# Optimization experiments

Measured on AMD Instinct MI355X. Metric: run time of the kernel, lower is better.

## Reference

```python
import jax, jax.numpy as jnp
import numpy as np

B, S, E, H = 1, 2048, 512, 8
D = E // H
N = B * S
WIN_HALF = 32  # attention_window 64 -> +/-32
ALPHA = 0.1
LN_EPS = 1e-12
NEG_INF = -1e9


def _build_window_edges():
    # windowed graph: dst i attends to src j with |i-j| <= WIN_HALF, within each batch block
    i = np.arange(S)
    offs = np.arange(-WIN_HALF, WIN_HALF + 1)
    src = i[:, None] + offs[None, :]
    dst = np.broadcast_to(i[:, None], src.shape)
    valid = (src >= 0) & (src < S)
    src, dst = src[valid], dst[valid]
    srcs, dsts = [], []
    for b in range(B):
        srcs.append(src + b * S)
        dsts.append(dst + b * S)
    return (np.concatenate(srcs).astype(np.int32),
            np.concatenate(dsts).astype(np.int32))


def setup_inputs() -> dict:
    key = jax.random.key(0)
    ks = jax.random.split(key, 12)
    sc = 1.0 / np.sqrt(E)
    src_np, dst_np = _build_window_edges()
    return {
        "hidden_states": jax.random.normal(ks[0], (B, S, E), dtype=jnp.float32),
        "attention_mask": jnp.zeros((B, S), dtype=jnp.float32),
        "edge_src": jnp.asarray(src_np),
        "edge_dst": jnp.asarray(dst_np),
        "Wq": jax.random.normal(ks[1], (E, E), dtype=jnp.float32) * sc,
        "bq": jnp.zeros((E,), dtype=jnp.float32),
        "Wk": jax.random.normal(ks[2], (E, E), dtype=jnp.float32) * sc,
        "bk": jnp.zeros((E,), dtype=jnp.float32),
        "Wv": jax.random.normal(ks[3], (E, E), dtype=jnp.float32) * sc,
        "bv": jnp.zeros((E,), dtype=jnp.float32),
        "Wo": jax.random.normal(ks[4], (E, E), dtype=jnp.float32) * sc,
        "bo": jnp.zeros((E,), dtype=jnp.float32),
        "ln_g": jnp.ones((E,), dtype=jnp.float32),
        "ln_b": jnp.zeros((E,), dtype=jnp.float32),
    }


def reference(hidden_states, attention_mask, edge_src, edge_dst,
              Wq, bq, Wk, bk, Wv, bv, Wo, bo, ln_g, ln_b):
    x = hidden_states  # (B,S,E); node ordering n = b*S + s (matches torch reshape)
    q = ((x @ Wq + bq) / jnp.sqrt(jnp.asarray(D, x.dtype))).reshape(N, H, D)
    k = (x @ Wk + bk).reshape(N, H, D)
    v = (x @ Wv + bv).reshape(N, H, D)

    mask = (attention_mask >= 0).reshape(N)  # bool per node

    # u_dot_v('k','q','score'): per-edge, per-head dot product
    score = jnp.einsum('ehd,ehd->eh', k[edge_src], q[edge_dst])  # (Eg,H)
    score = jnp.where(mask[edge_src][:, None], score, NEG_INF)

    # edge_softmax over incoming edges of each destination node
    smax = jax.ops.segment_max(score, edge_dst, num_segments=N)
    p = jnp.exp(score - smax[edge_dst])
    denom = jax.ops.segment_sum(p, edge_dst, num_segments=N)
    p = p / denom[edge_dst]  # (Eg,H)

    # 5 diffusion steps: h <- A h, blended with residual v (dropout off in eval)
    h = v
    for _ in range(5):
        m = h[edge_src] * p[:, :, None]                      # u_mul_e
        h = jax.ops.segment_sum(m, edge_dst, num_segments=N)  # sum('m','h')
        h = (1.0 - ALPHA) * h + ALPHA * v

    attn = h.reshape(B, S, E)

    # DiffuserSelfOutput: dense -> residual add -> LayerNorm
    y = attn @ Wo + bo + hidden_states
    mu = y.mean(-1, keepdims=True)
    var = ((y - mu) ** 2).mean(-1, keepdims=True)
    out = (y - mu) * jax.lax.rsqrt(var + LN_EPS) * ln_g + ln_b
    return out
```

## Files before the change

### kernel.cpp

```cpp
#include <hip/hip_runtime.h>
#include <math.h>

#define S_LEN 2048
#define E_DIM 512
#define NE (S_LEN * E_DIM)
#define H_NUM 8
#define WH 32
#define NOFF 65
#define PROW (H_NUM * NOFF)
#define PN (S_LEN * PROW)

typedef float f32x4 __attribute__((ext_vector_type(4)));
typedef short short8 __attribute__((ext_vector_type(8)));

__device__ __forceinline__ unsigned short f2bf(float f) {
    union { float f; unsigned u; } cv; cv.f = f;
    unsigned u = cv.u;
    u += 0x7fffu + ((u >> 16) & 1u);
    return (unsigned short)(u >> 16);
}
__device__ __forceinline__ unsigned pk2(float x, float y) {
    return (unsigned)f2bf(x) | ((unsigned)f2bf(y) << 16);
}

#define LGKM_BARRIER() do {                                   \
    __builtin_amdgcn_sched_barrier(0);                        \
    asm volatile("s_waitcnt lgkmcnt(0)" ::: "memory");        \
    __builtin_amdgcn_s_barrier();                             \
    __builtin_amdgcn_sched_barrier(0);                        \
} while (0)

__device__ __forceinline__ void mfma_gemm_f32(
    const float* __restrict__ A, const float* __restrict__ W,
    const float* __restrict__ bias, float* __restrict__ C,
    float scale, int m0, int n0)
{
    __shared__ unsigned short As[2][64 * 40];
    __shared__ unsigned short Bs[2][64 * 40];
    const int tid = threadIdx.x;
    const int lane = tid & 63, wave = tid >> 6;
    const int quad = lane >> 4, l16 = lane & 15;
    const int wr = (wave >> 1) * 32, wc = (wave & 1) * 32;
    const int ar = tid >> 2, ac = (tid & 3) * 8;
    const int bn = tid & 63, bk0 = (tid >> 6) * 8;

    f32x4 acc00 = {0.f,0.f,0.f,0.f}, acc01 = acc00, acc10 = acc00, acc11 = acc00;

    const float* Arow = A + (size_t)(m0 + ar) * E_DIM;

    float4 a0r[2], a1r[2];
    float  br[2][8];

#define QLOAD(s_, i_) do {                                                    \
        int kk_ = (i_) * 32;                                                  \
        a0r[s_] = *(const float4*)(Arow + kk_ + ac);                          \
        a1r[s_] = *(const float4*)(Arow + kk_ + ac + 4);                      \
        _Pragma("unroll")                                                     \
        for (int j_ = 0; j_ < 8; ++j_)                                        \
            br[s_][j_] = W[(size_t)(kk_ + bk0 + j_) * E_DIM + n0 + bn];       \
    } while (0)

#define QPACK(s_, b_) do {                                                    \
        uint4 ap_;                                                            \
        ap_.x = pk2(a0r[s_].x, a0r[s_].y); ap_.y = pk2(a0r[s_].z, a0r[s_].w); \
        ap_.z = pk2(a1r[s_].x, a1r[s_].y); ap_.w = pk2(a1r[s_].z, a1r[s_].w); \
        *(uint4*)(&As[b_][0] + ar * 40 + ac) = ap_;                           \
        uint4 bp_;                                                            \
        bp_.x = pk2(br[s_][0], br[s_][1]); bp_.y = pk2(br[s_][2], br[s_][3]); \
        bp_.z = pk2(br[s_][4], br[s_][5]); bp_.w = pk2(br[s_][6], br[s_][7]); \
        *(uint4*)(&Bs[b_][0] + bn * 40 + bk0) = bp_;                          \
    } while (0)

    QLOAD(0, 0);
    QPACK(0, 0);
    QLOAD(1, 1);
    LGKM_BARRIER();

#pragma unroll
    for (int it = 0; it < 16; ++it) {
        if (it < 14) QLOAD(it & 1, it + 2);

        const unsigned short* Ab = &As[it & 1][0];
        const unsigned short* Bb = &Bs[it & 1][0];
        short8 fa0 = *(const short8*)(Ab + (wr + l16) * 40 + quad * 8);
        short8 fa1 = *(const short8*)(Ab + (wr + 16 + l16) * 40 + quad * 8);
        short8 fb0 = *(const short8*)(Bb + (wc + l16) * 40 + quad * 8);
        short8 fb1 = *(const short8*)(Bb + (wc + 16 + l16) * 40 + quad * 8);
        acc00 = __builtin_amdgcn_mfma_f32_16x16x32_bf16(fa0, fb0, acc00, 0, 0, 0);
        acc01 = __builtin_amdgcn_mfma_f32_16x16x32_bf16(fa0, fb1, acc01, 0, 0, 0);
        acc10 = __builtin_amdgcn_mfma_f32_16x16x32_bf16(fa1, fb0, acc10, 0, 0, 0);
        acc11 = __builtin_amdgcn_mfma_f32_16x16x32_bf16(fa1, fb1, acc11, 0, 0, 0);

        if (it < 15) {
            QPACK((it + 1) & 1, (it + 1) & 1);
            LGKM_BARRIER();
        }
    }
#undef QLOAD
#undef QPACK

#pragma unroll
    for (int mi = 0; mi < 2; ++mi) {
#pragma unroll
        for (int ni = 0; ni < 2; ++ni) {
            f32x4 a = (mi == 0) ? ((ni == 0) ? acc00 : acc01)
                                : ((ni == 0) ? acc10 : acc11);
            int n = n0 + wc + ni * 16 + l16;
            float bval = bias[n];
#pragma unroll
            for (int r = 0; r < 4; ++r) {
                int m = m0 + wr + mi * 16 + quad * 4 + r;
                C[(size_t)m * E_DIM + n] = (a[r] + bval) * scale;
            }
        }
    }
}

__global__ __launch_bounds__(256)
void qkv_gemm(const float* __restrict__ x,
              const float* __restrict__ Wq, const float* __restrict__ bq,
              const float* __restrict__ Wk, const float* __restrict__ bk,
              const float* __restrict__ Wv, const float* __restrict__ bv,
              float* __restrict__ q, float* __restrict__ k, float* __restrict__ v)
{
    const float* W; const float* b; float* o; float sc;
    if (blockIdx.z == 0)      { W = Wq; b = bq; o = q; sc = 0.125f; }
    else if (blockIdx.z == 1) { W = Wk; b = bk; o = k; sc = 1.0f; }
    else                      { W = Wv; b = bv; o = v; sc = 1.0f; }
    mfma_gemm_f32(x, W, b, o, sc, blockIdx.y * 64, blockIdx.x * 64);
}

#define SDN 32
__global__ __launch_bounds__(256)
void scores_d1(const float* __restrict__ q, const float* __restrict__ k,
               const float* __restrict__ v, const float* __restrict__ amask,
               float* __restrict__ P, float* __restrict__ hA)
{
    const int i0 = blockIdx.x * SDN;
    const int h  = blockIdx.y;
    const int tid = threadIdx.x;
    __shared__ float ks[96 * 68];
    __shared__ float am[96];
    __shared__ float ps[SDN * NOFF];

    for (int e = tid; e < 96 * 16; e += 256) {
        int lr = e >> 4, c4 = e & 15;
        int j = i0 - WH + lr;
        int jc = min(max(j, 0), S_LEN - 1);
        *(float4*)(ks + lr * 68 + c4 * 4) =
            *(const float4*)(k + (size_t)jc * E_DIM + h * 64 + c4 * 4);
    }
    if (tid < 96) {
        int j = i0 - WH + tid;
        am[tid] = (j >= 0 && j < S_LEN) ? amask[j] : -1.0f;
    }

    const int dst = tid >> 3;
    const int og  = tid & 7;
    float4 qreg[16];
    {
        const float4* qrow = (const float4*)(q + (size_t)(i0 + dst) * E_DIM + h * 64);
#pragma unroll
        for (int t = 0; t < 16; ++t) qreg[t] = qrow[t];
    }
    __syncthreads();

    float sreg[9];
#pragma unroll
    for (int t = 0; t < 9; ++t) sreg[t] = -INFINITY;
#pragma unroll
    for (int t = 0; t < 9; ++t) {
        int off = og + 8 * t;
        if (off > 64) break;
        int j = i0 + dst + off - WH;
        if (j >= 0 && j < S_LEN) {
            int lr = dst + off;
            const float4* kr = (const float4*)(ks + lr * 68);
            float acc = 0.f;
#pragma unroll
            for (int u = 0; u < 16; ++u) {
                float4 a = qreg[u], bb = kr[u];
                acc += a.x * bb.x + a.y * bb.y + a.z * bb.z + a.w * bb.w;
            }
            sreg[t] = (am[lr] >= 0.f) ? acc : -1e9f;
        }
    }
    __syncthreads();

    for (int e = tid; e < 96 * 16; e += 256) {
        int lr = e >> 4, c4 = e & 15;
        int j = i0 - WH + lr;
        int jc = min(max(j, 0), S_LEN - 1);
        *(float4*)(ks + lr * 68 + c4 * 4) =
            *(const float4*)(v + (size_t)jc * E_DIM + h * 64 + c4 * 4);
    }

    float mx = sreg[0];
#pragma unroll
    for (int t = 1; t < 9; ++t) mx = fmaxf(mx, sreg[t]);
#pragma unroll
    for (int o = 1; o < 8; o <<= 1) mx = fmaxf(mx, __shfl_xor(mx, o, 64));
    float dn = 0.f;
#pragma unroll
    for (int t = 0; t < 9; ++t) {
        sreg[t] = expf(sreg[t] - mx);
        dn += sreg[t];
    }
#pragma unroll
    for (int o = 1; o < 8; o <<= 1) dn += __shfl_xor(dn, o, 64);
    float rinv = 1.f / dn;
#pragma unroll
    for (int t = 0; t < 9; ++t) {
        int off = og + 8 * t;
        if (off > 64) break;
        float pv = sreg[t] * rinv;
        P[(size_t)(i0 + dst) * PROW + h * NOFF + off] = pv;
        ps[dst * NOFF + off] = pv;
    }
    __syncthreads();

    {
        const int ci = tid & 15;
        const int ob = (tid >> 4) * 2;
        float4 a0 = {0,0,0,0}, a1 = a0;
        for (int lr = ob; lr < ob + 66; ++lr) {
            float4 hval = *(const float4*)(ks + lr * 68 + ci * 4);
            int o0 = lr - ob;
            if (o0 <= 64) {
                float p = ps[ob * NOFF + o0];
                a0.x += p * hval.x; a0.y += p * hval.y; a0.z += p * hval.z; a0.w += p * hval.w;
            }
            int o1 = o0 - 1;
            if ((unsigned)o1 <= 64u) {
                float p = ps[(ob + 1) * NOFF + o1];
                a1.x += p * hval.x; a1.y += p * hval.y; a1.z += p * hval.z; a1.w += p * hval.w;
            }
        }
#pragma unroll
        for (int r = 0; r < 2; ++r) {
            float4 a = r ? a1 : a0;
            float4 vv = *(const float4*)(ks + (WH + ob + r) * 68 + ci * 4);
            float4 o;
            o.x = 0.9f * a.x + 0.1f * vv.x;
            o.y = 0.9f * a.y + 0.1f * vv.y;
            o.z = 0.9f * a.z + 0.1f * vv.z;
            o.w = 0.9f * a.w + 0.1f * vv.w;
            *(float4*)(hA + (size_t)(i0 + ob + r) * E_DIM + h * 64 + ci * 4) = o;
        }
    }
}

__global__ __launch_bounds__(512)
void diffuse4m(const float* __restrict__ hin, const float* __restrict__ v,
               const float* __restrict__ P, unsigned short* __restrict__ h5b)
{
    __shared__ unsigned short inT[64 * 328];
    __shared__ unsigned short m1T[64 * 264];
    __shared__ unsigned short ps[256 * 66];
    unsigned short* m2T = inT;
    unsigned short* m3T = m1T;
    const int i0 = blockIdx.x * 64;
    const int h  = blockIdx.y;
    const int c0 = h * 64;
    const int tid  = threadIdx.x;
    const int lane = tid & 63, wave = tid >> 6;
    const int quad = lane >> 4, l16 = lane & 15;

    for (int e = tid; e < 160 * 16; e += 512) {
        int rp = (e >> 4) * 2, c4 = (e & 15) * 4;
        int ja = min(max(i0 - 128 + rp,     0), S_LEN - 1);
        int jb = min(max(i0 - 128 + rp + 1, 0), S_LEN - 1);
        float4 ha = *(const float4*)(hin + (size_t)ja * E_DIM + c0 + c4);
        float4 hb = *(const float4*)(hin + (size_t)jb * E_DIM + c0 + c4);
        *(unsigned*)(inT + (c4 + 0) * 328 + rp) = pk2(ha.x, hb.x);
        *(unsigned*)(inT + (c4 + 1) * 328 + rp) = pk2(ha.y, hb.y);
        *(unsigned*)(inT + (c4 + 2) * 328 + rp) = pk2(ha.z, hb.z);
        *(unsigned*)(inT + (c4 + 3) * 328 + rp) = pk2(ha.w, hb.w);
    }
    for (int e = tid; e < 256 * 33; e += 512) {
        int mr = e / 33, t = e - mr * 33;
        int jc = min(max(i0 - 96 + mr, 0), S_LEN - 1);
        const float* pr = P + (size_t)jc * PROW + h * NOFF;
        if (t < 32)
            *(unsigned*)(ps + mr * 66 + t * 2) = pk2(pr[t * 2], pr[t * 2 + 1]);
        else
            ps[mr * 66 + 64] = f2bf(pr[64]);
    }
    __syncthreads();

#pragma unroll
    for (int uu = 0; uu < 4; ++uu) {
        int u = wave + uu * 8;
        int mtb = (u >> 1) * 16;
        int ntb = (u & 1) * 32;
        f32x4 a0 = {0.f,0.f,0.f,0.f}, a1 = a0;
        int ks0 = mtb >> 5;
        const int m = mtb + l16;
#pragma unroll
        for (int t = 0; t < 3; ++t) {
            int k0q = (ks0 + t) * 32 + quad * 8;
            short8 fa;
#pragma unroll
            for (int j = 0; j < 8; ++j) {
                int idx = k0q + j - m;
                int idc = min(max(idx, 0), 64);
                unsigned short pv = ps[m * 66 + idc];
                fa[j] = ((unsigned)idx <= 64u) ? (short)pv : (short)0;
            }
            short8 fb0 = *(const short8*)(inT + (ntb + l16) * 328 + k0q);
            short8 fb1 = *(const short8*)(inT + (ntb + 16 + l16) * 328 + k0q);
            a0 = __builtin_amdgcn_mfma_f32_16x16x32_bf16(fa, fb0, a0, 0, 0, 0);
            a1 = __builtin_amdgcn_mfma_f32_16x16x32_bf16(fa, fb1, a1, 0, 0, 0);
        }
#pragma unroll
        for (int nt = 0; nt < 2; ++nt) {
            f32x4 a = nt ? a1 : a0;
            int n = ntb + nt * 16 + l16;
            float o[4];
#pragma unroll
            for (int r = 0; r < 4; ++r) {
                int gm = min(max(i0 - 96 + mtb + quad * 4 + r, 0), S_LEN - 1);
                o[r] = 0.9f * a[r] + 0.1f * v[(size_t)gm * E_DIM + c0 + n];
            }
            *(unsigned*)(m1T + n * 264 + mtb + quad * 4)     = pk2(o[0], o[1]);
            *(unsigned*)(m1T + n * 264 + mtb + quad * 4 + 2) = pk2(o[2], o[3]);
        }
    }
    __syncthreads();

#pragma unroll
    for (int uu = 0; uu < 3; ++uu) {
        int u = wave + uu * 8;
        int mtb = (u >> 1) * 16;
        int ntb = (u & 1) * 32;
        f32x4 a0 = {0.f,0.f,0.f,0.f}, a1 = a0;
        int ks0 = mtb >> 5;
        const int m = mtb + l16;
#pragma unroll
        for (int t = 0; t < 3; ++t) {
            int k0q = (ks0 + t) * 32 + quad * 8;
            short8 fa;
#pragma unroll
            for (int j = 0; j < 8; ++j) {
                int idx = k0q + j - m;
                int idc = min(max(idx, 0), 64);
                unsigned short pv = ps[(m + 32) * 66 + idc];
                fa[j] = ((unsigned)idx <= 64u) ? (short)pv : (short)0;
            }
            short8 fb0 = *(const short8*)(m1T + (ntb + l16) * 264 + k0q);
            short8 fb1 = *(const short8*)(m1T + (ntb + 16 + l16) * 264 + k0q);
            a0 = __builtin_amdgcn_mfma_f32_16x16x32_bf16(fa, fb0, a0, 0, 0, 0);
            a1 = __builtin_amdgcn_mfma_f32_16x16x32_bf16(fa, fb1, a1, 0, 0, 0);
        }
#pragma unroll
        for (int nt = 0; nt < 2; ++nt) {
            f32x4 a = nt ? a1 : a0;
            int n = ntb + nt * 16 + l16;
            float o[4];
#pragma unroll
            for (int r = 0; r < 4; ++r) {
                int gm = min(max(i0 - 64 + mtb + quad * 4 + r, 0), S_LEN - 1);
                o[r] = 0.9f * a[r] + 0.1f * v[(size_t)gm * E_DIM + c0 + n];
            }
            *(unsigned*)(m2T + n * 200 + mtb + quad * 4)     = pk2(o[0], o[1]);
            *(unsigned*)(m2T + n * 200 + mtb + quad * 4 + 2) = pk2(o[2], o[3]);
        }
    }
    __syncthreads();

#pragma unroll
    for (int uu = 0; uu < 2; ++uu) {
        int u = wave + uu * 8;
        int mtb = (u >> 1) * 16;
        int ntb = (u & 1) * 32;
        f32x4 a0 = {0.f,0.f,0.f,0.f}, a1 = a0;
        int ks0 = mtb >> 5;
        const int m = mtb + l16;
#pragma unroll
        for (int t = 0; t < 3; ++t) {
            int k0q = (ks0 + t) * 32 + quad * 8;
            short8 fa;
#pragma unroll
            for (int j = 0; j < 8; ++j) {
                int idx = k0q + j - m;
                int idc = min(max(idx, 0), 64);
                unsigned short pv = ps[(m + 64) * 66 + idc];
                fa[j] = ((unsigned)idx <= 64u) ? (short)pv : (short)0;
            }
            short8 fb0 = *(const short8*)(m2T + (ntb + l16) * 200 + k0q);
            short8 fb1 = *(const short8*)(m2T + (ntb + 16 + l16) * 200 + k0q);
            a0 = __builtin_amdgcn_mfma_f32_16x16x32_bf16(fa, fb0, a0, 0, 0, 0);
            a1 = __builtin_amdgcn_mfma_f32_16x16x32_bf16(fa, fb1, a1, 0, 0, 0);
        }
#pragma unroll
        for (int nt = 0; nt < 2; ++nt) {
            f32x4 a = nt ? a1 : a0;
            int n = ntb + nt * 16 + l16;
            float o[4];
#pragma unroll
            for (int r = 0; r < 4; ++r) {
                int gm = min(max(i0 - 32 + mtb + quad * 4 + r, 0), S_LEN - 1);
                o[r] = 0.9f * a[r] + 0.1f * v[(size_t)gm * E_DIM + c0 + n];
            }
            *(unsigned*)(m3T + n * 136 + mtb + quad * 4)     = pk2(o[0], o[1]);
            *(unsigned*)(m3T + n * 136 + mtb + quad * 4 + 2) = pk2(o[2], o[3]);
        }
    }
    __syncthreads();

    {
        int u = wave;
        int mtb = (u >> 1) * 16;
        int ntb = (u & 1) * 32;
        f32x4 a0 = {0.f,0.f,0.f,0.f}, a1 = a0;
        int ks0 = mtb >> 5;
        const int m = mtb + l16;
#pragma unroll
        for (int t = 0; t < 3; ++t) {
            int k0q = (ks0 + t) * 32 + quad * 8;
            short8 fa;
#pragma unroll
            for (int j = 0; j < 8; ++j) {
                int idx = k0q + j - m;
                int idc = min(max(idx, 0), 64);
                unsigned short pv = ps[(m + 96) * 66 + idc];
                fa[j] = ((unsigned)idx <= 64u) ? (short)pv : (short)0;
            }
            short8 fb0 = *(const short8*)(m3T + (ntb + l16) * 136 + k0q);
            short8 fb1 = *(const short8*)(m3T + (ntb + 16 + l16) * 136 + k0q);
            a0 = __builtin_amdgcn_mfma_f32_16x16x32_bf16(fa, fb0, a0, 0, 0, 0);
            a1 = __builtin_amdgcn_mfma_f32_16x16x32_bf16(fa, fb1, a1, 0, 0, 0);
        }
#pragma unroll
        for (int nt = 0; nt < 2; ++nt) {
            f32x4 a = nt ? a1 : a0;
            int n = ntb + nt * 16 + l16;
#pragma unroll
            for (int r = 0; r < 4; ++r) {
                int gm = i0 + mtb + quad * 4 + r;
                float vv = v[(size_t)gm * E_DIM + c0 + n];
                h5b[(size_t)gm * E_DIM + c0 + n] = f2bf(0.9f * a[r] + 0.1f * vv);
            }
        }
    }
}

__global__ __launch_bounds__(512)
void oln5(const unsigned short* __restrict__ h5b, const float* __restrict__ Wo,
          const float* __restrict__ bo, const float* __restrict__ x,
          const float* __restrict__ g, const float* __restrict__ lb,
          float* __restrict__ out)
{
    __shared__ unsigned short Bs2[2][512 * 40];
    __shared__ float rsum[8][16], rsq[8][16];
    const int tid = threadIdx.x;
    const int lane = tid & 63, wave = tid >> 6;
    const int quad = lane >> 4, l16 = lane & 15;
    const int m0 = blockIdx.x * 16;
    const int n = tid;

    short8 far_[16];
#pragma unroll
    for (int t = 0; t < 16; ++t)
        far_[t] = *(const short8*)(h5b + (size_t)(m0 + l16) * E_DIM + t * 32 + quad * 8);

    {
        float w0[32];
#pragma unroll
        for (int j = 0; j < 32; ++j)
            w0[j] = Wo[(size_t)j * E_DIM + n];
#pragma unroll
        for (int t = 0; t < 4; ++t) {
            uint4 bp;
            bp.x = pk2(w0[t*8+0], w0[t*8+1]); bp.y = pk2(w0[t*8+2], w0[t*8+3]);
            bp.z = pk2(w0[t*8+4], w0[t*8+5]); bp.w = pk2(w0[t*8+6], w0[t*8+7]);
            *(uint4*)(&Bs2[0][0] + n * 40 + t * 8) = bp;
        }
    }
    LGKM_BARRIER();

    f32x4 acc[4];
#pragma unroll
    for (int t = 0; t < 4; ++t) acc[t] = (f32x4){0.f,0.f,0.f,0.f};

#pragma unroll
    for (int it = 0; it < 16; ++it) {
        float wn[32];
        if (it < 15) {
#pragma unroll
            for (int j = 0; j < 32; ++j)
                wn[j] = Wo[(size_t)((it + 1) * 32 + j) * E_DIM + n];
        }

#pragma unroll
        for (int nt = 0; nt < 4; ++nt) {
            short8 fb = *(const short8*)(&Bs2[it & 1][0] +
                                         (wave * 64 + nt * 16 + l16) * 40 + quad * 8);
            acc[nt] = __builtin_amdgcn_mfma_f32_16x16x32_bf16(far_[it], fb, acc[nt], 0, 0, 0);
        }

        if (it < 15) {
#pragma unroll
            for (int t = 0; t < 4; ++t) {
                uint4 bp;
                bp.x = pk2(wn[t*8+0], wn[t*8+1]); bp.y = pk2(wn[t*8+2], wn[t*8+3]);
                bp.z = pk2(wn[t*8+4], wn[t*8+5]); bp.w = pk2(wn[t*8+6], wn[t*8+7]);
                *(uint4*)(&Bs2[(it + 1) & 1][0] + n * 40 + t * 8) = bp;
            }
            LGKM_BARRIER();
        }
    }

    float s[4] = {0.f,0.f,0.f,0.f}, s2[4] = {0.f,0.f,0.f,0.f};
#pragma unroll
    for (int nt = 0; nt < 4; ++nt) {
        int nc = wave * 64 + nt * 16 + l16;
        float bv = bo[nc];
#pragma unroll
        for (int r = 0; r < 4; ++r) {
            int m = m0 + quad * 4 + r;
            float vl = acc[nt][r] + bv + x[(size_t)m * E_DIM + nc];
            acc[nt][r] = vl;
            s[r] += vl; s2[r] += vl * vl;
        }
    }
#pragma unroll
    for (int o = 1; o < 16; o <<= 1) {
#pragma unroll
        for (int r = 0; r < 4; ++r) {
            s[r]  += __shfl_xor(s[r], o, 64);
            s2[r] += __shfl_xor(s2[r], o, 64);
        }
    }
    if (l16 == 0) {
#pragma unroll
        for (int r = 0; r < 4; ++r) {
            rsum[wave][quad * 4 + r] = s[r];
            rsq[wave][quad * 4 + r]  = s2[r];
        }
    }
    __syncthreads();
    float mu[4], rs[4];
#pragma unroll
    for (int r = 0; r < 4; ++r) {
        int rl = quad * 4 + r;
        float tot = 0.f, tot2 = 0.f;
#pragma unroll
        for (int w = 0; w < 8; ++w) { tot += rsum[w][rl]; tot2 += rsq[w][rl]; }
        float m_ = tot * (1.f / 512.f);
        float var = tot2 * (1.f / 512.f) - m_ * m_;
        mu[r] = m_; rs[r] = rsqrtf(var + 1e-12f);
    }
#pragma unroll
    for (int nt = 0; nt < 4; ++nt) {
        int nc = wave * 64 + nt * 16 + l16;
        float gv = g[nc], bbv = lb[nc];
#pragma unroll
        for (int r = 0; r < 4; ++r) {
            int m = m0 + quad * 4 + r;
            out[(size_t)m * E_DIM + nc] = (acc[nt][r] - mu[r]) * rs[r] * gv + bbv;
        }
    }
}

extern "C" void kernel_launch(void* const* d_in, const int* in_sizes, int n_in,
                              void* d_out, int out_size, void* d_ws, size_t ws_size,
                              hipStream_t stream)
{
    const float* x     = (const float*)d_in[0];
    const float* amask = (const float*)d_in[1];
    const float* Wq = (const float*)d_in[4];
    const float* bq = (const float*)d_in[5];
    const float* Wk = (const float*)d_in[6];
    const float* bk = (const float*)d_in[7];
    const float* Wv = (const float*)d_in[8];
    const float* bv = (const float*)d_in[9];
    const float* Wo = (const float*)d_in[10];
    const float* bo = (const float*)d_in[11];
    const float* lng = (const float*)d_in[12];
    const float* lnb = (const float*)d_in[13];
    float* out = (float*)d_out;

    float* ws = (float*)d_ws;
    float* q  = ws;
    float* k  = ws + (size_t)NE;
    float* v  = ws + (size_t)2 * NE;
    float* P  = ws + (size_t)3 * NE;
    float* hA = ws + (size_t)3 * NE + PN;
    unsigned short* h5b = (unsigned short*)(ws + (size_t)4 * NE + PN);

    qkv_gemm<<<dim3(8, 32, 3), 256, 0, stream>>>(x, Wq, bq, Wk, bk, Wv, bv, q, k, v);

    scores_d1<<<dim3(64, 8), 256, 0, stream>>>(q, k, v, amask, P, hA);

    diffuse4m<<<dim3(32, 8), 512, 0, stream>>>(hA, v, P, h5b);

    oln5<<<128, 512, 0, stream>>>(h5b, Wo, bo, x, lng, lnb, out);
}
```

Measured before the change: 164.4 us.

## Fuse all four stages into one cooperative persistent kernel with grid syncs

Replaces the four separate launches (QKV GEMM, scores plus first diffusion step, four-step diffusion, output projection with LayerNorm) with a single cooperative kernel of 256 blocks of 512 threads. Each block splits into two 256-thread halves that work on separate tiles, and the stages are separated by grid.sync. This removes the per-launch overhead and the gaps between kernels. In exchange it caps parallelism at 256 blocks with one block per CU, uses a large fixed shared-memory allocation, and adds the cost of the grid barriers themselves.

```diff
diff --git a/kernel.cpp b/kernel.cpp
--- a/kernel.cpp
+++ b/kernel.cpp
@@ -1,5 +1,8 @@
 #include <hip/hip_runtime.h>
+#include <hip/hip_cooperative_groups.h>
 #include <math.h>
+
+namespace cg = cooperative_groups;
 
 #define S_LEN 2048
 #define E_DIM 512
@@ -30,19 +33,18 @@
     __builtin_amdgcn_sched_barrier(0);                        \
 } while (0)
 
-__device__ __forceinline__ void mfma_gemm_f32(
+__device__ __forceinline__ void gemm64(
     const float* __restrict__ A, const float* __restrict__ W,
     const float* __restrict__ bias, float* __restrict__ C,
-    float scale, int m0, int n0)
+    float scale, int m0, int n0,
+    unsigned short* As, unsigned short* Bs, int htid, bool active)
 {
-    __shared__ unsigned short As[2][64 * 40];
-    __shared__ unsigned short Bs[2][64 * 40];
-    const int tid = threadIdx.x;
-    const int lane = tid & 63, wave = tid >> 6;
+    const int lane = htid & 63;
+    const int wave = (htid >> 6) & 3;
     const int quad = lane >> 4, l16 = lane & 15;
     const int wr = (wave >> 1) * 32, wc = (wave & 1) * 32;
-    const int ar = tid >> 2, ac = (tid & 3) * 8;
-    const int bn = tid & 63, bk0 = (tid >> 6) * 8;
+    const int ar = htid >> 2, ac = (htid & 3) * 8;
+    const int bn = htid & 63, bk0 = ((htid >> 6) & 3) * 8;
 
     f32x4 acc00 = {0.f,0.f,0.f,0.f}, acc01 = acc00, acc10 = acc00, acc11 = acc00;
 
@@ -64,11 +66,11 @@
         uint4 ap_;                                                            \
         ap_.x = pk2(a0r[s_].x, a0r[s_].y); ap_.y = pk2(a0r[s_].z, a0r[s_].w); \
         ap_.z = pk2(a1r[s_].x, a1r[s_].y); ap_.w = pk2(a1r[s_].z, a1r[s_].w); \
-        *(uint4*)(&As[b_][0] + ar * 40 + ac) = ap_;                           \
+        *(uint4*)(As + (b_) * 2560 + ar * 40 + ac) = ap_;                     \
         uint4 bp_;                                                            \
         bp_.x = pk2(br[s_][0], br[s_][1]); bp_.y = pk2(br[s_][2], br[s_][3]); \
         bp_.z = pk2(br[s_][4], br[s_][5]); bp_.w = pk2(br[s_][6], br[s_][7]); \
-        *(uint4*)(&Bs[b_][0] + bn * 40 + bk0) = bp_;                          \
+        *(uint4*)(Bs + (b_) * 2560 + bn * 40 + bk0) = bp_;                    \
     } while (0)
 
     QLOAD(0, 0);
@@ -80,8 +82,8 @@
     for (int it = 0; it < 16; ++it) {
         if (it < 14) QLOAD(it & 1, it + 2);
 
-        const unsigned short* Ab = &As[it & 1][0];
-        const unsigned short* Bb = &Bs[it & 1][0];
+        const unsigned short* Ab = As + (it & 1) * 2560;
+        const unsigned short* Bb = Bs + (it & 1) * 2560;
         short8 fa0 = *(const short8*)(Ab + (wr + l16) * 40 + quad * 8);
         short8 fa1 = *(const short8*)(Ab + (wr + 16 + l16) * 40 + quad * 8);
         short8 fb0 = *(const short8*)(Bb + (wc + l16) * 40 + quad * 8);
@@ -99,466 +101,485 @@
 #undef QLOAD
 #undef QPACK
 
-#pragma unroll
-    for (int mi = 0; mi < 2; ++mi) {
-#pragma unroll
-        for (int ni = 0; ni < 2; ++ni) {
-            f32x4 a = (mi == 0) ? ((ni == 0) ? acc00 : acc01)
-                                : ((ni == 0) ? acc10 : acc11);
-            int n = n0 + wc + ni * 16 + l16;
-            float bval = bias[n];
-#pragma unroll
-            for (int r = 0; r < 4; ++r) {
-                int m = m0 + wr + mi * 16 + quad * 4 + r;
-                C[(size_t)m * E_DIM + n] = (a[r] + bval) * scale;
+    if (active) {
+#pragma unroll
+        for (int mi = 0; mi < 2; ++mi) {
+#pragma unroll
+            for (int ni = 0; ni < 2; ++ni) {
+                f32x4 a = (mi == 0) ? ((ni == 0) ? acc00 : acc01)
+                                    : ((ni == 0) ? acc10 : acc11);
+                int n = n0 + wc + ni * 16 + l16;
+                float bval = bias[n];
+#pragma unroll
+                for (int r = 0; r < 4; ++r) {
+                    int m = m0 + wr + mi * 16 + quad * 4 + r;
+                    C[(size_t)m * E_DIM + n] = (a[r] + bval) * scale;
+                }
             }
         }
     }
 }
 
-__global__ __launch_bounds__(256)
-void qkv_gemm(const float* __restrict__ x,
-              const float* __restrict__ Wq, const float* __restrict__ bq,
-              const float* __restrict__ Wk, const float* __restrict__ bk,
-              const float* __restrict__ Wv, const float* __restrict__ bv,
-              float* __restrict__ q, float* __restrict__ k, float* __restrict__ v)
+__global__ __launch_bounds__(512, 1)
+void fused_all(const float* __restrict__ x, const float* __restrict__ amask,
+               const float* __restrict__ Wq, const float* __restrict__ bq,
+               const float* __restrict__ Wk, const float* __restrict__ bk,
+               const float* __restrict__ Wv, const float* __restrict__ bv,
+               const float* __restrict__ Wo, const float* __restrict__ bo,
+               const float* __restrict__ lng, const float* __restrict__ lnb,
+               float* __restrict__ out,
+               float* __restrict__ q, float* __restrict__ k, float* __restrict__ v,
+               float* __restrict__ P, float* __restrict__ hA,
+               unsigned short* __restrict__ h5b)
 {
-    const float* W; const float* b; float* o; float sc;
-    if (blockIdx.z == 0)      { W = Wq; b = bq; o = q; sc = 0.125f; }
-    else if (blockIdx.z == 1) { W = Wk; b = bk; o = k; sc = 1.0f; }
-    else                      { W = Wv; b = bv; o = v; sc = 1.0f; }
-    mfma_gemm_f32(x, W, b, o, sc, blockIdx.y * 64, blockIdx.x * 64);
-}
-
-#define SDN 32
-__global__ __launch_bounds__(256)
-void scores_d1(const float* __restrict__ q, const float* __restrict__ k,
-               const float* __restrict__ v, const float* __restrict__ amask,
-               float* __restrict__ P, float* __restrict__ hA)
-{
-    const int i0 = blockIdx.x * SDN;
-    const int h  = blockIdx.y;
-    const int tid = threadIdx.x;
-    __shared__ float ks[96 * 68];
-    __shared__ float am[96];
-    __shared__ float ps[SDN * NOFF];
-
-    for (int e = tid; e < 96 * 16; e += 256) {
-        int lr = e >> 4, c4 = e & 15;
-        int j = i0 - WH + lr;
-        int jc = min(max(j, 0), S_LEN - 1);
-        *(float4*)(ks + lr * 68 + c4 * 4) =
-            *(const float4*)(k + (size_t)jc * E_DIM + h * 64 + c4 * 4);
-    }
-    if (tid < 96) {
-        int j = i0 - WH + tid;
-        am[tid] = (j >= 0 && j < S_LEN) ? amask[j] : -1.0f;
-    }
-
-    const int dst = tid >> 3;
-    const int og  = tid & 7;
-    float4 qreg[16];
-    {
-        const float4* qrow = (const float4*)(q + (size_t)(i0 + dst) * E_DIM + h * 64);
-#pragma unroll
-        for (int t = 0; t < 16; ++t) qreg[t] = qrow[t];
-    }
-    __syncthreads();
-
-    float sreg[9];
-#pragma unroll
-    for (int t = 0; t < 9; ++t) sreg[t] = -INFINITY;
-#pragma unroll
-    for (int t = 0; t < 9; ++t) {
-        int off = og + 8 * t;
-        if (off > 64) break;
-        int j = i0 + dst + off - WH;
-        if (j >= 0 && j < S_LEN) {
-            int lr = dst + off;
-            const float4* kr = (const float4*)(ks + lr * 68);
-            float acc = 0.f;
-#pragma unroll
-            for (int u = 0; u < 16; ++u) {
-                float4 a = qreg[u], bb = kr[u];
-                acc += a.x * bb.x + a.y * bb.y + a.z * bb.z + a.w * bb.w;
-            }
-            sreg[t] = (am[lr] >= 0.f) ? acc : -1e9f;
-        }
-    }
-    __syncthreads();
-
-    for (int e = tid; e < 96 * 16; e += 256) {
-        int lr = e >> 4, c4 = e & 15;
-        int j = i0 - WH + lr;
-        int jc = min(max(j, 0), S_LEN - 1);
-        *(float4*)(ks + lr * 68 + c4 * 4) =
-            *(const float4*)(v + (size_t)jc * E_DIM + h * 64 + c4 * 4);
-    }
-
-    float mx = sreg[0];
-#pragma unroll
-    for (int t = 1; t < 9; ++t) mx = fmaxf(mx, sreg[t]);
-#pragma unroll
-    for (int o = 1; o < 8; o <<= 1) mx = fmaxf(mx, __shfl_xor(mx, o, 64));
-    float dn = 0.f;
-#pragma unroll
-    for (int t = 0; t < 9; ++t) {
-        sreg[t] = expf(sreg[t] - mx);
-        dn += sreg[t];
-    }
-#pragma unroll
-    for (int o = 1; o < 8; o <<= 1) dn += __shfl_xor(dn, o, 64);
-    float rinv = 1.f / dn;
-#pragma unroll
-    for (int t = 0; t < 9; ++t) {
-        int off = og + 8 * t;
-        if (off > 64) break;
-        float pv = sreg[t] * rinv;
-        P[(size_t)(i0 + dst) * PROW + h * NOFF + off] = pv;
-        ps[dst * NOFF + off] = pv;
-    }
-    __syncthreads();
-
-    {
-        const int ci = tid & 15;
-        const int ob = (tid >> 4) * 2;
-        float4 a0 = {0,0,0,0}, a1 = a0;
-        for (int lr = ob; lr < ob + 66; ++lr) {
-            float4 hval = *(const float4*)(ks + lr * 68 + ci * 4);
-            int o0 = lr - ob;
-            if (o0 <= 64) {
-                float p = ps[ob * NOFF + o0];
-                a0.x += p * hval.x; a0.y += p * hval.y; a0.z += p * hval.z; a0.w += p * hval.w;
-            }
-            int o1 = o0 - 1;
-            if ((unsigned)o1 <= 64u) {
-                float p = ps[(ob + 1) * NOFF + o1];
-                a1.x += p * hval.x; a1.y += p * hval.y; a1.z += p * hval.z; a1.w += p * hval.w;
-            }
-        }
-#pragma unroll
-        for (int r = 0; r < 2; ++r) {
-            float4 a = r ? a1 : a0;
-            float4 vv = *(const float4*)(ks + (WH + ob + r) * 68 + ci * 4);
-            float4 o;
-            o.x = 0.9f * a.x + 0.1f * vv.x;
-            o.y = 0.9f * a.y + 0.1f * vv.y;
-            o.z = 0.9f * a.z + 0.1f * vv.z;
-            o.w = 0.9f * a.w + 0.1f * vv.w;
-            *(float4*)(hA + (size_t)(i0 + ob + r) * E_DIM + h * 64 + ci * 4) = o;
-        }
-    }
-}
-
-__global__ __launch_bounds__(512)
-void diffuse4m(const float* __restrict__ hin, const float* __restrict__ v,
-               const float* __restrict__ P, unsigned short* __restrict__ h5b)
-{
-    __shared__ unsigned short inT[64 * 328];
-    __shared__ unsigned short m1T[64 * 264];
-    __shared__ unsigned short ps[256 * 66];
-    unsigned short* m2T = inT;
-    unsigned short* m3T = m1T;
-    const int i0 = blockIdx.x * 64;
-    const int h  = blockIdx.y;
-    const int c0 = h * 64;
+    __shared__ __align__(16) unsigned char smem[110592];
+    cg::grid_group grid = cg::this_grid();
+
     const int tid  = threadIdx.x;
+    const int bid  = blockIdx.x;
+    const int half = tid >> 8;
+    const int htid = tid & 255;
     const int lane = tid & 63, wave = tid >> 6;
     const int quad = lane >> 4, l16 = lane & 15;
 
-    for (int e = tid; e < 160 * 16; e += 512) {
-        int rp = (e >> 4) * 2, c4 = (e & 15) * 4;
-        int ja = min(max(i0 - 128 + rp,     0), S_LEN - 1);
-        int jb = min(max(i0 - 128 + rp + 1, 0), S_LEN - 1);
-        float4 ha = *(const float4*)(hin + (size_t)ja * E_DIM + c0 + c4);
-        float4 hb = *(const float4*)(hin + (size_t)jb * E_DIM + c0 + c4);
-        *(unsigned*)(inT + (c4 + 0) * 328 + rp) = pk2(ha.x, hb.x);
-        *(unsigned*)(inT + (c4 + 1) * 328 + rp) = pk2(ha.y, hb.y);
-        *(unsigned*)(inT + (c4 + 2) * 328 + rp) = pk2(ha.z, hb.z);
-        *(unsigned*)(inT + (c4 + 3) * 328 + rp) = pk2(ha.w, hb.w);
+    {
+        unsigned short* As = (unsigned short*)(smem + half * 20480);
+        unsigned short* Bs = As + 2 * 2560;
+#pragma unroll
+        for (int it = 0; it < 2; ++it) {
+            int u = it * 512 + bid * 2 + half;
+            bool active = (u < 768);
+            int uc = active ? u : 767;
+            int z  = uc >> 8;
+            int mt = (uc >> 3) & 31;
+            int nt = uc & 7;
+            const float* W; const float* b; float* o; float sc;
+            if (z == 0)      { W = Wq; b = bq; o = q; sc = 0.125f; }
+            else if (z == 1) { W = Wk; b = bk; o = k; sc = 1.0f; }
+            else             { W = Wv; b = bv; o = v; sc = 1.0f; }
+            gemm64(x, W, b, o, sc, mt * 64, nt * 64, As, Bs, htid, active);
+        }
     }
-    for (int e = tid; e < 256 * 33; e += 512) {
-        int mr = e / 33, t = e - mr * 33;
-        int jc = min(max(i0 - 96 + mr, 0), S_LEN - 1);
-        const float* pr = P + (size_t)jc * PROW + h * NOFF;
-        if (t < 32)
-            *(unsigned*)(ps + mr * 66 + t * 2) = pk2(pr[t * 2], pr[t * 2 + 1]);
-        else
-            ps[mr * 66 + 64] = f2bf(pr[64]);
+    __threadfence();
+    grid.sync();
+
+    {
+        unsigned char* hb = smem + half * 34816;
+        float* ks = (float*)hb;
+        float* am = (float*)(hb + 26112);
+        float* ps = (float*)(hb + 26496);
+        int u = bid * 2 + half;
+        const int i0 = (u >> 3) * 32;
+        const int h  = u & 7;
+
+        for (int e = htid; e < 96 * 16; e += 256) {
+            int lr = e >> 4, c4 = e & 15;
+            int j = i0 - WH + lr;
+            int jc = min(max(j, 0), S_LEN - 1);
+            *(float4*)(ks + lr * 68 + c4 * 4) =
+                *(const float4*)(k + (size_t)jc * E_DIM + h * 64 + c4 * 4);
+        }
+        if (htid < 96) {
+            int j = i0 - WH + htid;
+            am[htid] = (j >= 0 && j < S_LEN) ? amask[j] : -1.0f;
+        }
+
+        const int dst = htid >> 3;
+        const int og  = htid & 7;
+        float4 qreg[16];
+        {
+            const float4* qrow = (const float4*)(q + (size_t)(i0 + dst) * E_DIM + h * 64);
+#pragma unroll
+            for (int t = 0; t < 16; ++t) qreg[t] = qrow[t];
+        }
+        __syncthreads();
+
+        float sreg[9];
+#pragma unroll
+        for (int t = 0; t < 9; ++t) sreg[t] = -INFINITY;
+#pragma unroll
+        for (int t = 0; t < 9; ++t) {
+            int off = og + 8 * t;
+            if (off > 64) break;
+            int j = i0 + dst + off - WH;
+            if (j >= 0 && j < S_LEN) {
+                int lr = dst + off;
+                const float4* kr = (const float4*)(ks + lr * 68);
+                float acc = 0.f;
+#pragma unroll
+                for (int uu = 0; uu < 16; ++uu) {
+                    float4 a = qreg[uu], bb = kr[uu];
+                    acc += a.x * bb.x + a.y * bb.y + a.z * bb.z + a.w * bb.w;
+                }
+                sreg[t] = (am[lr] >= 0.f) ? acc : -1e9f;
+            }
+        }
+        __syncthreads();
+
+        for (int e = htid; e < 96 * 16; e += 256) {
+            int lr = e >> 4, c4 = e & 15;
+            int j = i0 - WH + lr;
+            int jc = min(max(j, 0), S_LEN - 1);
+            *(float4*)(ks + lr * 68 + c4 * 4) =
+                *(const float4*)(v + (size_t)jc * E_DIM + h * 64 + c4 * 4);
+        }
+
+        float mx = sreg[0];
+#pragma unroll
+        for (int t = 1; t < 9; ++t) mx = fmaxf(mx, sreg[t]);
+#pragma unroll
+        for (int o = 1; o < 8; o <<= 1) mx = fmaxf(mx, __shfl_xor(mx, o, 64));
+        float dn = 0.f;
+#pragma unroll
+        for (int t = 0; t < 9; ++t) {
+            sreg[t] = expf(sreg[t] - mx);
+            dn += sreg[t];
+        }
+#pragma unroll
+        for (int o = 1; o < 8; o <<= 1) dn += __shfl_xor(dn, o, 64);
+        float rinv = 1.f / dn;
+#pragma unroll
+        for (int t = 0; t < 9; ++t) {
+            int off = og + 8 * t;
+            if (off > 64) break;
+            float pv = sreg[t] * rinv;
+            P[(size_t)(i0 + dst) * PROW + h * NOFF + off] = pv;
+            ps[dst * NOFF + off] = pv;
+        }
+        __syncthreads();
+
+        {
+            const int ci = htid & 15;
+            const int ob = (htid >> 4) * 2;
+            float4 a0 = {0,0,0,0}, a1 = a0;
+            for (int lr = ob; lr < ob + 66; ++lr) {
+                float4 hval = *(const float4*)(ks + lr * 68 + ci * 4);
+                int o0 = lr - ob;
+                if (o0 <= 64) {
+                    float p = ps[ob * NOFF + o0];
+                    a0.x += p * hval.x; a0.y += p * hval.y; a0.z += p * hval.z; a0.w += p * hval.w;
+                }
+                int o1 = o0 - 1;
+                if ((unsigned)o1 <= 64u) {
+                    float p = ps[(ob + 1) * NOFF + o1];
+                    a1.x += p * hval.x; a1.y += p * hval.y; a1.z += p * hval.z; a1.w += p * hval.w;
+                }
+            }
+#pragma unroll
+            for (int r = 0; r < 2; ++r) {
+                float4 a = r ? a1 : a0;
+                float4 vv = *(const float4*)(ks + (WH + ob + r) * 68 + ci * 4);
+                float4 o;
+                o.x = 0.9f * a.x + 0.1f * vv.x;
+                o.y = 0.9f * a.y + 0.1f * vv.y;
+                o.z = 0.9f * a.z + 0.1f * vv.z;
+                o.w = 0.9f * a.w + 0.1f * vv.w;
+                *(float4*)(hA + (size_t)(i0 + ob + r) * E_DIM + h * 64 + ci * 4) = o;
+            }
+        }
     }
-    __syncthreads();
-
-#pragma unroll
-    for (int uu = 0; uu < 4; ++uu) {
-        int u = wave + uu * 8;
-        int mtb = (u >> 1) * 16;
-        int ntb = (u & 1) * 32;
-        f32x4 a0 = {0.f,0.f,0.f,0.f}, a1 = a0;
-        int ks0 = mtb >> 5;
-        const int m = mtb + l16;
-#pragma unroll
-        for (int t = 0; t < 3; ++t) {
-            int k0q = (ks0 + t) * 32 + quad * 8;
-            short8 fa;
-#pragma unroll
-            for (int j = 0; j < 8; ++j) {
-                int idx = k0q + j - m;
-                int idc = min(max(idx, 0), 64);
-                unsigned short pv = ps[m * 66 + idc];
-                fa[j] = ((unsigned)idx <= 64u) ? (short)pv : (short)0;
-            }
-            short8 fb0 = *(const short8*)(inT + (ntb + l16) * 328 + k0q);
-            short8 fb1 = *(const short8*)(inT + (ntb + 16 + l16) * 328 + k0q);
-            a0 = __builtin_amdgcn_mfma_f32_16x16x32_bf16(fa, fb0, a0, 0, 0, 0);
-            a1 = __builtin_amdgcn_mfma_f32_16x16x32_bf16(fa, fb1, a1, 0, 0, 0);
-        }
-#pragma unroll
-        for (int nt = 0; nt < 2; ++nt) {
-            f32x4 a = nt ? a1 : a0;
-            int n = ntb + nt * 16 + l16;
-            float o[4];
-#pragma unroll
-            for (int r = 0; r < 4; ++r) {
-                int gm = min(max(i0 - 96 + mtb + quad * 4 + r, 0), S_LEN - 1);
-                o[r] = 0.9f * a[r] + 0.1f * v[(size_t)gm * E_DIM + c0 + n];
-            }
-            *(unsigned*)(m1T + n * 264 + mtb + quad * 4)     = pk2(o[0], o[1]);
-            *(unsigned*)(m1T + n * 264 + mtb + quad * 4 + 2) = pk2(o[2], o[3]);
+    __threadfence();
+    grid.sync();
+
+    {
+        unsigned short* inT = (unsigned short*)smem;
+        unsigned short* m1T = (unsigned short*)(smem + 41984);
+        unsigned short* ps  = (unsigned short*)(smem + 75776);
+        unsigned short* m2T = inT;
+        unsigned short* m3T = m1T;
+        const int i0 = (bid >> 3) * 64;
+        const int h  = bid & 7;
+        const int c0 = h * 64;
+
+        for (int e = tid; e < 160 * 16; e += 512) {
+            int rp = (e >> 4) * 2, c4 = (e & 15) * 4;
+            int ja = min(max(i0 - 128 + rp,     0), S_LEN - 1);
+            int jb = min(max(i0 - 128 + rp + 1, 0), S_LEN - 1);
+            float4 ha = *(const float4*)(hA + (size_t)ja * E_DIM + c0 + c4);
+            float4 hb2 = *(const float4*)(hA + (size_t)jb * E_DIM + c0 + c4);
+            *(unsigned*)(inT + (c4 + 0) * 328 + rp) = pk2(ha.x, hb2.x);
+            *(unsigned*)(inT + (c4 + 1) * 328 + rp) = pk2(ha.y, hb2.y);
+            *(unsigned*)(inT + (c4 + 2) * 328 + rp) = pk2(ha.z, hb2.z);
+            *(unsigned*)(inT + (c4 + 3) * 328 + rp) = pk2(ha.w, hb2.w);
+        }
+        for (int e = tid; e < 256 * 33; e += 512) {
+            int mr = e / 33, t = e - mr * 33;
+            int jc = min(max(i0 - 96 + mr, 0), S_LEN - 1);
+            const float* pr = P + (size_t)jc * PROW + h * NOFF;
+            if (t < 32)
+                *(unsigned*)(ps + mr * 66 + t * 2) = pk2(pr[t * 2], pr[t * 2 + 1]);
+            else
+                ps[mr * 66 + 64] = f2bf(pr[64]);
+        }
+        __syncthreads();
+
+#pragma unroll
+        for (int uu = 0; uu < 4; ++uu) {
+            int u = wave + uu * 8;
+            int mtb = (u >> 1) * 16;
+            int ntb = (u & 1) * 32;
+            f32x4 a0 = {0.f,0.f,0.f,0.f}, a1 = a0;
+            int ks0 = mtb >> 5;
+            const int m = mtb + l16;
+#pragma unroll
+            for (int t = 0; t < 3; ++t) {
+                int k0q = (ks0 + t) * 32 + quad * 8;
+                short8 fa;
+#pragma unroll
+                for (int j = 0; j < 8; ++j) {
+                    int idx = k0q + j - m;
+                    int idc = min(max(idx, 0), 64);
+                    unsigned short pv = ps[m * 66 + idc];
+                    fa[j] = ((unsigned)idx <= 64u) ? (short)pv : (short)0;
+                }
+                short8 fb0 = *(const short8*)(inT + (ntb + l16) * 328 + k0q);
+                short8 fb1 = *(const short8*)(inT + (ntb + 16 + l16) * 328 + k0q);
+                a0 = __builtin_amdgcn_mfma_f32_16x16x32_bf16(fa, fb0, a0, 0, 0, 0);
+                a1 = __builtin_amdgcn_mfma_f32_16x16x32_bf16(fa, fb1, a1, 0, 0, 0);
+            }
+#pragma unroll
+            for (int nt = 0; nt < 2; ++nt) {
+                f32x4 a = nt ? a1 : a0;
+                int n = ntb + nt * 16 + l16;
+                float o[4];
+#pragma unroll
+                for (int r = 0; r < 4; ++r) {
+                    int gm = min(max(i0 - 96 + mtb + quad * 4 + r, 0), S_LEN - 1);
+                    o[r] = 0.9f * a[r] + 0.1f * v[(size_t)gm * E_DIM + c0 + n];
+                }
+                *(unsigned*)(m1T + n * 264 + mtb + quad * 4)     = pk2(o[0], o[1]);
+                *(unsigned*)(m1T + n * 264 + mtb + quad * 4 + 2) = pk2(o[2], o[3]);
+            }
+        }
+        __syncthreads();
+
+#pragma unroll
+        for (int uu = 0; uu < 3; ++uu) {
+            int u = wave + uu * 8;
+            int mtb = (u >> 1) * 16;
+            int ntb = (u & 1) * 32;
+            f32x4 a0 = {0.f,0.f,0.f,0.f}, a1 = a0;
+            int ks0 = mtb >> 5;
+            const int m = mtb + l16;
+#pragma unroll
+            for (int t = 0; t < 3; ++t) {
+                int k0q = (ks0 + t) * 32 + quad * 8;
+                short8 fa;
+#pragma unroll
+                for (int j = 0; j < 8; ++j) {
+                    int idx = k0q + j - m;
+                    int idc = min(max(idx, 0), 64);
+                    unsigned short pv = ps[(m + 32) * 66 + idc];
+                    fa[j] = ((unsigned)idx <= 64u) ? (short)pv : (short)0;
+                }
+                short8 fb0 = *(const short8*)(m1T + (ntb + l16) * 264 + k0q);
+                short8 fb1 = *(const short8*)(m1T + (ntb + 16 + l16) * 264 + k0q);
+                a0 = __builtin_amdgcn_mfma_f32_16x16x32_bf16(fa, fb0, a0, 0, 0, 0);
+                a1 = __builtin_amdgcn_mfma_f32_16x16x32_bf16(fa, fb1, a1, 0, 0, 0);
+            }
+#pragma unroll
+            for (int nt = 0; nt < 2; ++nt) {
+                f32x4 a = nt ? a1 : a0;
+                int n = ntb + nt * 16 + l16;
+                float o[4];
+#pragma unroll
+                for (int r = 0; r < 4; ++r) {
+                    int gm = min(max(i0 - 64 + mtb + quad * 4 + r, 0), S_LEN - 1);
+                    o[r] = 0.9f * a[r] + 0.1f * v[(size_t)gm * E_DIM + c0 + n];
+                }
+                *(unsigned*)(m2T + n * 200 + mtb + quad * 4)     = pk2(o[0], o[1]);
+                *(unsigned*)(m2T + n * 200 + mtb + quad * 4 + 2) = pk2(o[2], o[3]);
+            }
+        }
+        __syncthreads();
+
+#pragma unroll
+        for (int uu = 0; uu < 2; ++uu) {
+            int u = wave + uu * 8;
+            int mtb = (u >> 1) * 16;
+            int ntb = (u & 1) * 32;
+            f32x4 a0 = {0.f,0.f,0.f,0.f}, a1 = a0;
+            int ks0 = mtb >> 5;
+            const int m = mtb + l16;
+#pragma unroll
+            for (int t = 0; t < 3; ++t) {
+                int k0q = (ks0 + t) * 32 + quad * 8;
+                short8 fa;
+#pragma unroll
+                for (int j = 0; j < 8; ++j) {
+                    int idx = k0q + j - m;
+                    int idc = min(max(idx, 0), 64);
+                    unsigned short pv = ps[(m + 64) * 66 + idc];
+                    fa[j] = ((unsigned)idx <= 64u) ? (short)pv : (short)0;
+                }
+                short8 fb0 = *(const short8*)(m2T + (ntb + l16) * 200 + k0q);
+                short8 fb1 = *(const short8*)(m2T + (ntb + 16 + l16) * 200 + k0q);
+                a0 = __builtin_amdgcn_mfma_f32_16x16x32_bf16(fa, fb0, a0, 0, 0, 0);
+                a1 = __builtin_amdgcn_mfma_f32_16x16x32_bf16(fa, fb1, a1, 0, 0, 0);
+            }
+#pragma unroll
+            for (int nt = 0; nt < 2; ++nt) {
+                f32x4 a = nt ? a1 : a0;
+                int n = ntb + nt * 16 + l16;
+                float o[4];
+#pragma unroll
+                for (int r = 0; r < 4; ++r) {
+                    int gm = min(max(i0 - 32 + mtb + quad * 4 + r, 0), S_LEN - 1);
+                    o[r] = 0.9f * a[r] + 0.1f * v[(size_t)gm * E_DIM + c0 + n];
+                }
+                *(unsigned*)(m3T + n * 136 + mtb + quad * 4)     = pk2(o[0], o[1]);
+                *(unsigned*)(m3T + n * 136 + mtb + quad * 4 + 2) = pk2(o[2], o[3]);
+            }
+        }
+        __syncthreads();
+
+        {
+            int u = wave;
+            int mtb = (u >> 1) * 16;
+            int ntb = (u & 1) * 32;
+            f32x4 a0 = {0.f,0.f,0.f,0.f}, a1 = a0;
+            int ks0 = mtb >> 5;
+            const int m = mtb + l16;
+#pragma unroll
+            for (int t = 0; t < 3; ++t) {
+                int k0q = (ks0 + t) * 32 + quad * 8;
+                short8 fa;
+#pragma unroll
+                for (int j = 0; j < 8; ++j) {
+                    int idx = k0q + j - m;
+                    int idc = min(max(idx, 0), 64);
+                    unsigned short pv = ps[(m + 96) * 66 + idc];
+                    fa[j] = ((unsigned)idx <= 64u) ? (short)pv : (short)0;
+                }
+                short8 fb0 = *(const short8*)(m3T + (ntb + l16) * 136 + k0q);
+                short8 fb1 = *(const short8*)(m3T + (ntb + 16 + l16) * 136 + k0q);
+                a0 = __builtin_amdgcn_mfma_f32_16x16x32_bf16(fa, fb0, a0, 0, 0, 0);
+                a1 = __builtin_amdgcn_mfma_f32_16x16x32_bf16(fa, fb1, a1, 0, 0, 0);
+            }
+#pragma unroll
+            for (int nt = 0; nt < 2; ++nt) {
+                f32x4 a = nt ? a1 : a0;
+                int n = ntb + nt * 16 + l16;
+#pragma unroll
+                for (int r = 0; r < 4; ++r) {
+                    int gm = i0 + mtb + quad * 4 + r;
+                    float vv = v[(size_t)gm * E_DIM + c0 + n];
+                    h5b[(size_t)gm * E_DIM + c0 + n] = f2bf(0.9f * a[r] + 0.1f * vv);
+                }
+            }
         }
     }
-    __syncthreads();
-
-#pragma unroll
-    for (int uu = 0; uu < 3; ++uu) {
-        int u = wave + uu * 8;
-        int mtb = (u >> 1) * 16;
-        int ntb = (u & 1) * 32;
-        f32x4 a0 = {0.f,0.f,0.f,0.f}, a1 = a0;
-        int ks0 = mtb >> 5;
-        const int m = mtb + l16;
-#pragma unroll
-        for (int t = 0; t < 3; ++t) {
-            int k0q = (ks0 + t) * 32 + quad * 8;
-            short8 fa;
-#pragma unroll
-            for (int j = 0; j < 8; ++j) {
-                int idx = k0q + j - m;
-                int idc = min(max(idx, 0), 64);
-                unsigned short pv = ps[(m + 32) * 66 + idc];
-                fa[j] = ((unsigned)idx <= 64u) ? (short)pv : (short)0;
-            }
-            short8 fb0 = *(const short8*)(m1T + (ntb + l16) * 264 + k0q);
-            short8 fb1 = *(const short8*)(m1T + (ntb + 16 + l16) * 264 + k0q);
-            a0 = __builtin_amdgcn_mfma_f32_16x16x32_bf16(fa, fb0, a0, 0, 0, 0);
-            a1 = __builtin_amdgcn_mfma_f32_16x16x32_bf16(fa, fb1, a1, 0, 0, 0);
-        }
-#pragma unroll
-        for (int nt = 0; nt < 2; ++nt) {
-            f32x4 a = nt ? a1 : a0;
-            int n = ntb + nt * 16 + l16;
-            float o[4];
-#pragma unroll
-            for (int r = 0; r < 4; ++r) {
-                int gm = min(max(i0 - 64 + mtb + quad * 4 + r, 0), S_LEN - 1);
-                o[r] = 0.9f * a[r] + 0.1f * v[(size_t)gm * E_DIM + c0 + n];
-            }
-            *(unsigned*)(m2T + n * 200 + mtb + quad * 4)     = pk2(o[0], o[1]);
-            *(unsigned*)(m2T + n * 200 + mtb + quad * 4 + 2) = pk2(o[2], o[3]);
-        }
-    }
-    __syncthreads();
-
-#pragma unroll
-    for (int uu = 0; uu < 2; ++uu) {
-        int u = wave + uu * 8;
-        int mtb = (u >> 1) * 16;
-        int ntb = (u & 1) * 32;
-        f32x4 a0 = {0.f,0.f,0.f,0.f}, a1 = a0;
-        int ks0 = mtb >> 5;
-        const int m = mtb + l16;
-#pragma unroll
-        for (int t = 0; t < 3; ++t) {
-            int k0q = (ks0 + t) * 32 + quad * 8;
-            short8 fa;
-#pragma unroll
-            for (int j = 0; j < 8; ++j) {
-                int idx = k0q + j - m;
-                int idc = min(max(idx, 0), 64);
-                unsigned short pv = ps[(m + 64) * 66 + idc];
-                fa[j] = ((unsigned)idx <= 64u) ? (short)pv : (short)0;
-            }
-            short8 fb0 = *(const short8*)(m2T + (ntb + l16) * 200 + k0q);
-            short8 fb1 = *(const short8*)(m2T + (ntb + 16 + l16) * 200 + k0q);
-            a0 = __builtin_amdgcn_mfma_f32_16x16x32_bf16(fa, fb0, a0, 0, 0, 0);
-            a1 = __builtin_amdgcn_mfma_f32_16x16x32_bf16(fa, fb1, a1, 0, 0, 0);
-        }
-#pragma unroll
-        for (int nt = 0; nt < 2; ++nt) {
-            f32x4 a = nt ? a1 : a0;
-            int n = ntb + nt * 16 + l16;
-            float o[4];
-#pragma unroll
-            for (int r = 0; r < 4; ++r) {
-                int gm = min(max(i0 - 32 + mtb + quad * 4 + r, 0), S_LEN - 1);
-                o[r] = 0.9f * a[r] + 0.1f * v[(size_t)gm * E_DIM + c0 + n];
-            }
-            *(unsigned*)(m3T + n * 136 + mtb + quad * 4)     = pk2(o[0], o[1]);
-            *(unsigned*)(m3T + n * 136 + mtb + quad * 4 + 2) = pk2(o[2], o[3]);
-        }
-    }
-    __syncthreads();
-
-    {
-        int u = wave;
-        int mtb = (u >> 1) * 16;
-        int ntb = (u & 1) * 32;
-        f32x4 a0 = {0.f,0.f,0.f,0.f}, a1 = a0;
-        int ks0 = mtb >> 5;
-        const int m = mtb + l16;
-#pragma unroll
-        for (int t = 0; t < 3; ++t) {
-            int k0q = (ks0 + t) * 32 + quad * 8;
-            short8 fa;
-#pragma unroll
-            for (int j = 0; j < 8; ++j) {
-                int idx = k0q + j - m;
-                int idc = min(max(idx, 0), 64);
-                unsigned short pv = ps[(m + 96) * 66 + idc];
-                fa[j] = ((unsigned)idx <= 64u) ? (short)pv : (short)0;
-            }
-            short8 fb0 = *(const short8*)(m3T + (ntb + l16) * 136 + k0q);
-            short8 fb1 = *(const short8*)(m3T + (ntb + 16 + l16) * 136 + k0q);
-            a0 = __builtin_amdgcn_mfma_f32_16x16x32_bf16(fa, fb0, a0, 0, 0, 0);
-            a1 = __builtin_amdgcn_mfma_f32_16x16x32_bf16(fa, fb1, a1, 0, 0, 0);
-        }
-#pragma unroll
-        for (int nt = 0; nt < 2; ++nt) {
-            f32x4 a = nt ? a1 : a0;
-            int n = ntb + nt * 16 + l16;
-#pragma unroll
-            for (int r = 0; r < 4; ++r) {
-                int gm = i0 + mtb + quad * 4 + r;
-                float vv = v[(size_t)gm * E_DIM + c0 + n];
-                h5b[(size_t)gm * E_DIM + c0 + n] = f2bf(0.9f * a[r] + 0.1f * vv);
-            }
-        }
-    }
-}
-
-__global__ __launch_bounds__(512)
-void oln5(const unsigned short* __restrict__ h5b, const float* __restrict__ Wo,
-          const float* __restrict__ bo, const float* __restrict__ x,
-          const float* __restrict__ g, const float* __restrict__ lb,
-          float* __restrict__ out)
-{
-    __shared__ unsigned short Bs2[2][512 * 40];
-    __shared__ float rsum[8][16], rsq[8][16];
-    const int tid = threadIdx.x;
-    const int lane = tid & 63, wave = tid >> 6;
-    const int quad = lane >> 4, l16 = lane & 15;
-    const int m0 = blockIdx.x * 16;
-    const int n = tid;
-
-    short8 far_[16];
-#pragma unroll
-    for (int t = 0; t < 16; ++t)
-        far_[t] = *(const short8*)(h5b + (size_t)(m0 + l16) * E_DIM + t * 32 + quad * 8);
-
-    {
-        float w0[32];
-#pragma unroll
-        for (int j = 0; j < 32; ++j)
-            w0[j] = Wo[(size_t)j * E_DIM + n];
-#pragma unroll
-        for (int t = 0; t < 4; ++t) {
-            uint4 bp;
-            bp.x = pk2(w0[t*8+0], w0[t*8+1]); bp.y = pk2(w0[t*8+2], w0[t*8+3]);
-            bp.z = pk2(w0[t*8+4], w0[t*8+5]); bp.w = pk2(w0[t*8+6], w0[t*8+7]);
-            *(uint4*)(&Bs2[0][0] + n * 40 + t * 8) = bp;
-        }
-    }
-    LGKM_BARRIER();
-
-    f32x4 acc[4];
-#pragma unroll
-    for (int t = 0; t < 4; ++t) acc[t] = (f32x4){0.f,0.f,0.f,0.f};
-
-#pragma unroll
-    for (int it = 0; it < 16; ++it) {
-        float wn[32];
-        if (it < 15) {
+    __threadfence();
+    grid.sync();
+
+    if (bid < 128) {
+        unsigned short* Bs2 = (unsigned short*)smem;
+        float* rsum = (float*)(smem + 81920);
+        float* rsq  = (float*)(smem + 81920 + 512);
+        const int m0 = bid * 16;
+        const int n = tid;
+
+        short8 far_[16];
+#pragma unroll
+        for (int t = 0; t < 16; ++t)
+            far_[t] = *(const short8*)(h5b + (size_t)(m0 + l16) * E_DIM + t * 32 + quad * 8);
+
+        {
+            float w0[32];
 #pragma unroll
             for (int j = 0; j < 32; ++j)
-                wn[j] = Wo[(size_t)((it + 1) * 32 + j) * E_DIM + n];
-        }
-
-#pragma unroll
-        for (int nt = 0; nt < 4; ++nt) {
-            short8 fb = *(const short8*)(&Bs2[it & 1][0] +
-                                         (wave * 64 + nt * 16 + l16) * 40 + quad * 8);
-            acc[nt] = __builtin_amdgcn_mfma_f32_16x16x32_bf16(far_[it], fb, acc[nt], 0, 0, 0);
-        }
-
-        if (it < 15) {
+                w0[j] = Wo[(size_t)j * E_DIM + n];
 #pragma unroll
             for (int t = 0; t < 4; ++t) {
                 uint4 bp;
-                bp.x = pk2(wn[t*8+0], wn[t*8+1]); bp.y = pk2(wn[t*8+2], wn[t*8+3]);
-                bp.z = pk2(wn[t*8+4], wn[t*8+5]); bp.w = pk2(wn[t*8+6], wn[t*8+7]);
-                *(uint4*)(&Bs2[(it + 1) & 1][0] + n * 40 + t * 8) = bp;
-            }
-            LGKM_BARRIER();
-        }
-    }
-
-    float s[4] = {0.f,0.f,0.f,0.f}, s2[4] = {0.f,0.f,0.f,0.f};
-#pragma unroll
-    for (int nt = 0; nt < 4; ++nt) {
-        int nc = wave * 64 + nt * 16 + l16;
-        float bv = bo[nc];
+                bp.x = pk2(w0[t*8+0], w0[t*8+1]); bp.y = pk2(w0[t*8+2], w0[t*8+3]);
+                bp.z = pk2(w0[t*8+4], w0[t*8+5]); bp.w = pk2(w0[t*8+6], w0[t*8+7]);
+                *(uint4*)(Bs2 + n * 40 + t * 8) = bp;
+            }
+        }
+        LGKM_BARRIER();
+
+        f32x4 acc[4];
+#pragma unroll
+        for (int t = 0; t < 4; ++t) acc[t] = (f32x4){0.f,0.f,0.f,0.f};
+
+#pragma unroll
+        for (int it = 0; it < 16; ++it) {
+            float wn[32];
+            if (it < 15) {
+#pragma unroll
+                for (int j = 0; j < 32; ++j)
+                    wn[j] = Wo[(size_t)((it + 1) * 32 + j) * E_DIM + n];
+            }
+
+#pragma unroll
+            for (int nt = 0; nt < 4; ++nt) {
+                short8 fb = *(const short8*)(Bs2 + (it & 1) * 20480 +
+                                             (wave * 64 + nt * 16 + l16) * 40 + quad * 8);
+                acc[nt] = __builtin_amdgcn_mfma_f32_16x16x32_bf16(far_[it], fb, acc[nt], 0, 0, 0);
+            }
+
+            if (it < 15) {
+#pragma unroll
+                for (int t = 0; t < 4; ++t) {
+                    uint4 bp;
+                    bp.x = pk2(wn[t*8+0], wn[t*8+1]); bp.y = pk2(wn[t*8+2], wn[t*8+3]);
+                    bp.z = pk2(wn[t*8+4], wn[t*8+5]); bp.w = pk2(wn[t*8+6], wn[t*8+7]);
+                    *(uint4*)(Bs2 + ((it + 1) & 1) * 20480 + n * 40 + t * 8) = bp;
+                }
+                LGKM_BARRIER();
+            }
+        }
+
+        float s[4] = {0.f,0.f,0.f,0.f}, s2[4] = {0.f,0.f,0.f,0.f};
+#pragma unroll
+        for (int nt = 0; nt < 4; ++nt) {
+            int nc = wave * 64 + nt * 16 + l16;
+            float bv = bo[nc];
+#pragma unroll
+            for (int r = 0; r < 4; ++r) {
+                int m = m0 + quad * 4 + r;
+                float vl = acc[nt][r] + bv + x[(size_t)m * E_DIM + nc];
+                acc[nt][r] = vl;
+                s[r] += vl; s2[r] += vl * vl;
+            }
+        }
+#pragma unroll
+        for (int o = 1; o < 16; o <<= 1) {
+#pragma unroll
+            for (int r = 0; r < 4; ++r) {
+                s[r]  += __shfl_xor(s[r], o, 64);
+                s2[r] += __shfl_xor(s2[r], o, 64);
+            }
+        }
+        if (l16 == 0) {
+#pragma unroll
+            for (int r = 0; r < 4; ++r) {
+                rsum[wave * 16 + quad * 4 + r] = s[r];
+                rsq[wave * 16 + quad * 4 + r]  = s2[r];
+            }
+        }
+        __syncthreads();
+        float mu[4], rs[4];
 #pragma unroll
         for (int r = 0; r < 4; ++r) {
-            int m = m0 + quad * 4 + r;
-            float vl = acc[nt][r] + bv + x[(size_t)m * E_DIM + nc];
-            acc[nt][r] = vl;
-            s[r] += vl; s2[r] += vl * vl;
-        }
-    }
-#pragma unroll
-    for (int o = 1; o < 16; o <<= 1) {
-#pragma unroll
-        for (int r = 0; r < 4; ++r) {
-            s[r]  += __shfl_xor(s[r], o, 64);
-            s2[r] += __shfl_xor(s2[r], o, 64);
-        }
-    }
-    if (l16 == 0) {
-#pragma unroll
-        for (int r = 0; r < 4; ++r) {
-            rsum[wave][quad * 4 + r] = s[r];
-            rsq[wave][quad * 4 + r]  = s2[r];
-        }
-    }
-    __syncthreads();
-    float mu[4], rs[4];
-#pragma unroll
-    for (int r = 0; r < 4; ++r) {
-        int rl = quad * 4 + r;
-        float tot = 0.f, tot2 = 0.f;
-#pragma unroll
-        for (int w = 0; w < 8; ++w) { tot += rsum[w][rl]; tot2 += rsq[w][rl]; }
-        float m_ = tot * (1.f / 512.f);
-        float var = tot2 * (1.f / 512.f) - m_ * m_;
-        mu[r] = m_; rs[r] = rsqrtf(var + 1e-12f);
-    }
-#pragma unroll
-    for (int nt = 0; nt < 4; ++nt) {
-        int nc = wave * 64 + nt * 16 + l16;
-        float gv = g[nc], bbv = lb[nc];
-#pragma unroll
-        for (int r = 0; r < 4; ++r) {
-            int m = m0 + quad * 4 + r;
-            out[(size_t)m * E_DIM + nc] = (acc[nt][r] - mu[r]) * rs[r] * gv + bbv;
+            int rl = quad * 4 + r;
+            float tot = 0.f, tot2 = 0.f;
+#pragma unroll
+            for (int w = 0; w < 8; ++w) { tot += rsum[w * 16 + rl]; tot2 += rsq[w * 16 + rl]; }
+            float m_ = tot * (1.f / 512.f);
+            float var = tot2 * (1.f / 512.f) - m_ * m_;
+            mu[r] = m_; rs[r] = rsqrtf(var + 1e-12f);
+        }
+#pragma unroll
+        for (int nt = 0; nt < 4; ++nt) {
+            int nc = wave * 64 + nt * 16 + l16;
+            float gv = lng[nc], bbv = lnb[nc];
+#pragma unroll
+            for (int r = 0; r < 4; ++r) {
+                int m = m0 + quad * 4 + r;
+                out[(size_t)m * E_DIM + nc] = (acc[nt][r] - mu[r]) * rs[r] * gv + bbv;
+            }
         }
     }
 }
@@ -589,11 +610,13 @@
     float* hA = ws + (size_t)3 * NE + PN;
     unsigned short* h5b = (unsigned short*)(ws + (size_t)4 * NE + PN);
 
-    qkv_gemm<<<dim3(8, 32, 3), 256, 0, stream>>>(x, Wq, bq, Wk, bk, Wv, bv, q, k, v);
-
-    scores_d1<<<dim3(64, 8), 256, 0, stream>>>(q, k, v, amask, P, hA);
-
-    diffuse4m<<<dim3(32, 8), 512, 0, stream>>>(hA, v, P, h5b);
-
-    oln5<<<128, 512, 0, stream>>>(h5b, Wo, bo, x, lng, lnb, out);
+    void* kargs[] = {
+        (void*)&x, (void*)&amask,
+        (void*)&Wq, (void*)&bq, (void*)&Wk, (void*)&bk, (void*)&Wv, (void*)&bv,
+        (void*)&Wo, (void*)&bo, (void*)&lng, (void*)&lnb,
+        (void*)&out,
+        (void*)&q, (void*)&k, (void*)&v, (void*)&P, (void*)&hA, (void*)&h5b
+    };
+    hipLaunchCooperativeKernel((const void*)fused_all, dim3(256), dim3(512),
+                               kargs, 0, stream);
 }
```

New measurement: 427.3 us. 2.6x slower.
